# Performance work log

Measured on AMD Instinct MI355X. Metric: run time of the kernel, lower is better.

Reference implementation:

```python
import jax, jax.numpy as jnp
import numpy as np
import math

ALPHA = math.exp(-0.001 * 1000.0)  # exp(-dt * tau_filter_inv)
T, B, D_IN, D_OUT = 2048, 32, 512, 512


def setup_inputs() -> dict:
    key = jax.random.key(0)
    k1, k2, k3 = jax.random.split(key, 3)
    bound = 1.0 / math.sqrt(D_IN)  # torch Linear default init range
    return {
        "input_tensor": jax.random.normal(k1, (T, B, D_IN), dtype=jnp.float32),
        "weight": jax.random.uniform(k2, (D_OUT, D_IN), minval=-bound, maxval=bound, dtype=jnp.float32),
        "bias": jax.random.uniform(k3, (D_OUT,), minval=-bound, maxval=bound, dtype=jnp.float32),
    }


def reference(input_tensor, weight, bias):
    # y[t] = W x[t] + b   -> [T, B, D_OUT]
    y = jnp.einsum("tbi,oi->tbo", input_tensor, weight) + bias
    alpha = jnp.asarray(ALPHA, dtype=y.dtype)

    # out[0] = y[0]; out[t] = alpha * out[t-1] + y[t]
    def step(carry, yt):
        out = alpha * carry + yt
        return out, out

    _, rest = jax.lax.scan(step, y[0], y[1:])
    return jnp.concatenate([y[:1], rest], axis=0)
```

## Files before the change

kernel.cpp:

```cpp
#include <hip/hip_runtime.h>
#include <stdint.h>

#define T_DIM 2048
#define B_DIM 32
#define DIN   512
#define DOUT  512
#define M_DIM (T_DIM * B_DIM)
#define COLS  (B_DIM * DIN)
#define COLS4 (COLS / 4)

#define ALPHA_F 0.36787944117144233f
#define INV_1MA 1.5819767068693265f

#define CHUNKS   128
#define CHUNK_T  16
#define HALO     8

#define FCHUNKS  32
#define FCHUNK_T 64
#define FHALO    16

typedef float  floatx4 __attribute__((ext_vector_type(4)));
typedef __bf16 bf16x8  __attribute__((ext_vector_type(8)));

__device__ __forceinline__ uint32_t pk2(float a, float b) {
  uint32_t ua = __float_as_uint(a); ua += 0x7fffu + ((ua >> 16) & 1u);
  uint32_t ub = __float_as_uint(b); ub += 0x7fffu + ((ub >> 16) & 1u);
  return (ua >> 16) | (ub & 0xffff0000u);
}

__device__ __forceinline__ void gload_lds16(const void* g, void* lds) {
  __builtin_amdgcn_global_load_lds(
      (const __attribute__((address_space(1))) void*)g,
      (__attribute__((address_space(3))) void*)lds,
      16, 0, 0);
}

__device__ __forceinline__ void fma4(float4& c, const float4& v) {
  c.x = fmaf(ALPHA_F, c.x, v.x);
  c.y = fmaf(ALPHA_F, c.y, v.y);
  c.z = fmaf(ALPHA_F, c.z, v.z);
  c.w = fmaf(ALPHA_F, c.w, v.w);
}

__global__ void wconv_kernel(const float* __restrict__ W,
                             uint16_t* __restrict__ WB)
{
  const int t = blockIdx.x * 256 + threadIdx.x;
  const float4* W4 = (const float4*)W;
#pragma unroll
  for (int j = 0; j < 8; ++j) {
    const int b4 = t * 16 + j * 2;
    float4 w0 = W4[b4], w1 = W4[b4 + 1];
    uint4 p;
    p.x = pk2(w0.x, w0.y); p.y = pk2(w0.z, w0.w);
    p.z = pk2(w1.x, w1.y); p.w = pk2(w1.z, w1.w);
    *(uint4*)&WB[t * 64 + j * 8] = p;
  }
}

__global__ void filter_x_kernel(const float* __restrict__ X,
                                uint16_t* __restrict__ XF)
{
  const int col8 = blockIdx.x * 256 + threadIdx.x;
  const int c = blockIdx.y;
  const float4* X4 = (const float4*)X;

  const size_t cbase = (size_t)c * CHUNK_T * COLS4 + col8 * 2;

  float4 ca = {0.0f, 0.0f, 0.0f, 0.0f};
  float4 cb = {0.0f, 0.0f, 0.0f, 0.0f};

  if (c > 0) {
    float4 h[2 * HALO];
    const size_t hb = cbase - (size_t)HALO * COLS4;
#pragma unroll
    for (int j = 0; j < HALO; ++j) {
      h[2 * j]     = X4[hb + (size_t)j * COLS4];
      h[2 * j + 1] = X4[hb + (size_t)j * COLS4 + 1];
    }
#pragma unroll
    for (int j = 0; j < HALO; ++j) {
      fma4(ca, h[2 * j]);
      fma4(cb, h[2 * j + 1]);
    }
  }

  float4 cur[8], nxt[8];
#pragma unroll
  for (int j = 0; j < 4; ++j) {
    cur[2 * j]     = X4[cbase + (size_t)j * COLS4];
    cur[2 * j + 1] = X4[cbase + (size_t)j * COLS4 + 1];
  }
#pragma unroll
  for (int g = 0; g < 4; ++g) {
    if (g < 3) {
      const size_t nb = cbase + (size_t)((g + 1) * 4) * COLS4;
#pragma unroll
      for (int j = 0; j < 4; ++j) {
        nxt[2 * j]     = X4[nb + (size_t)j * COLS4];
        nxt[2 * j + 1] = X4[nb + (size_t)j * COLS4 + 1];
      }
    }
#pragma unroll
    for (int j = 0; j < 4; ++j) {
      fma4(ca, cur[2 * j]);
      fma4(cb, cur[2 * j + 1]);
      uint4 p;
      p.x = pk2(ca.x, ca.y); p.y = pk2(ca.z, ca.w);
      p.z = pk2(cb.x, cb.y); p.w = pk2(cb.z, cb.w);
      *(uint4*)&XF[(cbase + (size_t)(g * 4 + j) * COLS4) * 4] = p;
    }
#pragma unroll
    for (int j = 0; j < 8; ++j) cur[j] = nxt[j];
  }
}

__launch_bounds__(256, 4)
__global__ void gemm_bf16_kernel(const uint16_t* __restrict__ XF,
                                 const uint16_t* __restrict__ WB,
                                 const float* __restrict__ bias,
                                 float* __restrict__ Y)
{
  __shared__ __align__(16) uint16_t As[128 * 64];
  __shared__ __align__(16) uint16_t Bs[128 * 64];

  const int bid = blockIdx.x;
  const int lg = (bid & 7) * 256 + (bid >> 3);
  const int n0 = (lg & 3) * 128;
  const int m0 = (lg >> 2) * 128;

  const int tid  = threadIdx.x;
  const int lane = tid & 63;
  const int w    = tid >> 6;
  const int r    = lane & 15;
  const int q    = lane >> 4;
  const int wm   = w >> 1;
  const int wn   = w & 1;

  const int srow_base = w * 32 + (lane >> 3);
  const int schunk    = lane & 7;

  floatx4 acc[4][4];
#pragma unroll
  for (int i = 0; i < 4; ++i)
#pragma unroll
    for (int j = 0; j < 4; ++j) {
      floatx4 z = {0.0f, 0.0f, 0.0f, 0.0f};
      acc[i][j] = z;
    }

  for (int kt = 0; kt < DIN / 64; ++kt) {
    const int k0 = kt * 64;
#pragma unroll
    for (int i = 0; i < 4; ++i) {
      const int row = srow_base + i * 8;
      const int sc = schunk ^ (row & 7);
      gload_lds16(XF + (size_t)(m0 + row) * DIN + k0 + sc * 8,
                  &As[(w * 32 + i * 8) * 64]);
      gload_lds16(WB + (size_t)(n0 + row) * DIN + k0 + sc * 8,
                  &Bs[(w * 32 + i * 8) * 64]);
    }
    __syncthreads();

#pragma unroll
    for (int kk = 0; kk < 2; ++kk) {
      bf16x8 af[4], bfr[4];
#pragma unroll
      for (int mi = 0; mi < 4; ++mi) {
        const int row = wm * 64 + mi * 16 + r;
        const int cch = (kk * 4 + q) ^ (row & 7);
        af[mi] = *(const bf16x8*)&As[row * 64 + (cch << 3)];
      }
#pragma unroll
      for (int ni = 0; ni < 4; ++ni) {
        const int row = wn * 64 + ni * 16 + r;
        const int cch = (kk * 4 + q) ^ (row & 7);
        bfr[ni] = *(const bf16x8*)&Bs[row * 64 + (cch << 3)];
      }
#pragma unroll
      for (int mi = 0; mi < 4; ++mi)
#pragma unroll
        for (int ni = 0; ni < 4; ++ni)
          acc[mi][ni] = __builtin_amdgcn_mfma_f32_16x16x32_bf16(
              af[mi], bfr[ni], acc[mi][ni], 0, 0, 0);
    }
    __syncthreads();
  }

#pragma unroll
  for (int mi = 0; mi < 4; ++mi) {
    const int rowb = m0 + wm * 64 + mi * 16;
    const int t = rowb >> 5;
    const float s = (1.0f - __expf(-(float)(t + 1))) * INV_1MA;
#pragma unroll
    for (int ni = 0; ni < 4; ++ni) {
      const int col = n0 + wn * 64 + ni * 16 + r;
      const float sb = s * bias[col];
#pragma unroll
      for (int j = 0; j < 4; ++j)
        Y[(size_t)(rowb + q * 4 + j) * DOUT + col] = acc[mi][ni][j] + sb;
    }
  }
}

__launch_bounds__(256, 2)
__global__ void gemm_bias_kernel(const float* __restrict__ X,
                                 const float* __restrict__ W,
                                 const float* __restrict__ bias,
                                 float* __restrict__ Y,
                                 float* __restrict__ halo,
                                 int halo_on)
{
  __shared__ __align__(16) uint16_t As[128 * 64];
  __shared__ __align__(16) uint16_t Bs[128 * 64];

  const int tid  = threadIdx.x;
  const int lane = tid & 63;
  const int wave = tid >> 6;
  const int wm   = wave >> 1;
  const int wn   = wave & 1;
  const int r    = lane & 15;
  const int q    = lane >> 4;

  const int m0 = blockIdx.y * 128;
  const int n0 = blockIdx.x * 128;

  floatx4 acc[4][4];
#pragma unroll
  for (int i = 0; i < 4; ++i)
#pragma unroll
    for (int j = 0; j < 4; ++j) {
      floatx4 z = {0.0f, 0.0f, 0.0f, 0.0f};
      acc[i][j] = z;
    }

  for (int kt = 0; kt < DIN / 64; ++kt) {
    const int k0 = kt * 64;
#pragma unroll
    for (int j = 0; j < 4; ++j) {
      const int cid = tid + j * 256;
      const int row = cid >> 3;
      const int c   = cid & 7;
      const int slot = (c ^ (row & 7)) << 3;

      const float* ga = &X[(size_t)(m0 + row) * DIN + k0 + c * 8];
      float4 a0 = *(const float4*)ga;
      float4 a1 = *(const float4*)(ga + 4);
      uint4 pa;
      pa.x = pk2(a0.x, a0.y); pa.y = pk2(a0.z, a0.w);
      pa.z = pk2(a1.x, a1.y); pa.w = pk2(a1.z, a1.w);
      *(uint4*)&As[row * 64 + slot] = pa;

      const float* gb = &W[(size_t)(n0 + row) * DIN + k0 + c * 8];
      float4 b0 = *(const float4*)gb;
      float4 b1 = *(const float4*)(gb + 4);
      uint4 pb;
      pb.x = pk2(b0.x, b0.y); pb.y = pk2(b0.z, b0.w);
      pb.z = pk2(b1.x, b1.y); pb.w = pk2(b1.z, b1.w);
      *(uint4*)&Bs[row * 64 + slot] = pb;
    }
    __syncthreads();

#pragma unroll
    for (int kk = 0; kk < 2; ++kk) {
      bf16x8 af[4], bfr[4];
#pragma unroll
      for (int mi = 0; mi < 4; ++mi) {
        const int row = wm * 64 + mi * 16 + r;
        const int c   = (kk * 4 + q) ^ (row & 7);
        af[mi] = *(const bf16x8*)&As[row * 64 + (c << 3)];
      }
#pragma unroll
      for (int ni = 0; ni < 4; ++ni) {
        const int row = wn * 64 + ni * 16 + r;
        const int c   = (kk * 4 + q) ^ (row & 7);
        bfr[ni] = *(const bf16x8*)&Bs[row * 64 + (c << 3)];
      }
#pragma unroll
      for (int mi = 0; mi < 4; ++mi)
#pragma unroll
        for (int ni = 0; ni < 4; ++ni)
          acc[mi][ni] = __builtin_amdgcn_mfma_f32_16x16x32_bf16(
              af[mi], bfr[ni], acc[mi][ni], 0, 0, 0);
    }
    __syncthreads();
  }

#pragma unroll
  for (int ni = 0; ni < 4; ++ni) {
    const int col = n0 + wn * 64 + ni * 16 + r;
    const float bv = bias[col];
#pragma unroll
    for (int mi = 0; mi < 4; ++mi) {
      const int rowm = m0 + wm * 64 + mi * 16 + q * 4;
      const int t = rowm >> 5;
      const int b = rowm & 31;
      const int tloc = t & (FCHUNK_T - 1);
      const bool hw = halo_on && (tloc >= FCHUNK_T - FHALO) && (t < T_DIM - FCHUNK_T);
      const size_t hbase = hw
          ? ((size_t)(((t >> 6) + 1) * FHALO + (tloc - (FCHUNK_T - FHALO))) * COLS)
          : 0;
#pragma unroll
      for (int j = 0; j < 4; ++j) {
        const float v = acc[mi][ni][j] + bv;
        Y[(size_t)(rowm + j) * DOUT + col] = v;
        if (hw) halo[hbase + (size_t)(b + j) * DOUT + col] = v;
      }
    }
  }
}

__global__ void scan_kernel(float* __restrict__ Y,
                            const float* __restrict__ halo,
                            int chunk_len)
{
  const int col4 = blockIdx.x * blockDim.x + threadIdx.x;
  const int c = blockIdx.y;

  float4* Y4 = (float4*)Y;
  const float4* H4 = (const float4*)halo;

  float4 carry = {0.0f, 0.0f, 0.0f, 0.0f};
  if (c > 0) {
#pragma unroll
    for (int h = 0; h < FHALO; ++h) {
      float4 v = H4[(size_t)(c * FHALO + h) * COLS4 + col4];
      fma4(carry, v);
    }
  }

  size_t idx = (size_t)c * chunk_len * COLS4 + col4;
  float4 ynext = Y4[idx];
  for (int t = 0; t < chunk_len; ++t) {
    float4 y = ynext;
    if (t + 1 < chunk_len) ynext = Y4[idx + COLS4];
    fma4(carry, y);
    Y4[idx] = carry;
    idx += COLS4;
  }
}

extern "C" void kernel_launch(void* const* d_in, const int* in_sizes, int n_in,
                              void* d_out, int out_size, void* d_ws, size_t ws_size,
                              hipStream_t stream)
{
  const float* X    = (const float*)d_in[0];
  const float* W    = (const float*)d_in[1];
  const float* bias = (const float*)d_in[2];
  float* Y = (float*)d_out;

  const size_t need_new = (size_t)M_DIM * DIN * 2 + (size_t)DOUT * DIN * 2;

  if (ws_size >= need_new) {
    uint16_t* XF = (uint16_t*)d_ws;
    uint16_t* WB = XF + (size_t)M_DIM * DIN;

    wconv_kernel<<<16, 256, 0, stream>>>(W, WB);
    dim3 gf(8, CHUNKS);
    filter_x_kernel<<<gf, 256, 0, stream>>>(X, XF);
    gemm_bf16_kernel<<<2048, 256, 0, stream>>>(XF, WB, bias, Y);
  } else {
    float* halo = (float*)d_ws;
    const size_t halo_need = (size_t)FCHUNKS * FHALO * COLS * sizeof(float);
    const int halo_on = (ws_size >= halo_need) ? 1 : 0;

    dim3 g1(DOUT / 128, M_DIM / 128);
    gemm_bias_kernel<<<g1, 256, 0, stream>>>(X, W, bias, Y, halo, halo_on);

    const int n_chunks = halo_on ? FCHUNKS : 1;
    dim3 g2(COLS4 / 256, n_chunks);
    scan_kernel<<<g2, 256, 0, stream>>>(Y, halo, T_DIM / n_chunks);
  }
}
```

Before: 107.6 us.

## Fuse input filtering into GEMM with per-batch time slabs

Replaces the separate filter pass (which wrote a bf16 filtered copy of X to workspace) and the GEMM with one fused kernel. Each block handles one batch index and a 256-step time slab: it filters X into a full-K LDS tile of 128 rows, then sweeps all output columns with double-buffered weight tiles. This removes the global write and re-read of the filtered intermediate. In exchange it uses only 256 blocks with one block per CU because of the large LDS footprint, and each thread issues strided X loads, so occupancy and latency hiding may suffer.

```diff
diff --git a/kernel.cpp b/kernel.cpp
--- a/kernel.cpp
+++ b/kernel.cpp
@@ -12,9 +12,9 @@
 #define ALPHA_F 0.36787944117144233f
 #define INV_1MA 1.5819767068693265f
 
-#define CHUNKS   128
-#define CHUNK_T  16
-#define HALO     8
+#define HALO   8
+#define TSLAB  256
+#define NSLABS 8
 
 #define FCHUNKS  32
 #define FCHUNK_T 64
@@ -59,76 +59,19 @@
   }
 }
 
-__global__ void filter_x_kernel(const float* __restrict__ X,
-                                uint16_t* __restrict__ XF)
-{
-  const int col8 = blockIdx.x * 256 + threadIdx.x;
-  const int c = blockIdx.y;
-  const float4* X4 = (const float4*)X;
-
-  const size_t cbase = (size_t)c * CHUNK_T * COLS4 + col8 * 2;
-
-  float4 ca = {0.0f, 0.0f, 0.0f, 0.0f};
-  float4 cb = {0.0f, 0.0f, 0.0f, 0.0f};
-
-  if (c > 0) {
-    float4 h[2 * HALO];
-    const size_t hb = cbase - (size_t)HALO * COLS4;
-#pragma unroll
-    for (int j = 0; j < HALO; ++j) {
-      h[2 * j]     = X4[hb + (size_t)j * COLS4];
-      h[2 * j + 1] = X4[hb + (size_t)j * COLS4 + 1];
-    }
-#pragma unroll
-    for (int j = 0; j < HALO; ++j) {
-      fma4(ca, h[2 * j]);
-      fma4(cb, h[2 * j + 1]);
-    }
-  }
-
-  float4 cur[8], nxt[8];
-#pragma unroll
-  for (int j = 0; j < 4; ++j) {
-    cur[2 * j]     = X4[cbase + (size_t)j * COLS4];
-    cur[2 * j + 1] = X4[cbase + (size_t)j * COLS4 + 1];
-  }
-#pragma unroll
-  for (int g = 0; g < 4; ++g) {
-    if (g < 3) {
-      const size_t nb = cbase + (size_t)((g + 1) * 4) * COLS4;
-#pragma unroll
-      for (int j = 0; j < 4; ++j) {
-        nxt[2 * j]     = X4[nb + (size_t)j * COLS4];
-        nxt[2 * j + 1] = X4[nb + (size_t)j * COLS4 + 1];
-      }
-    }
-#pragma unroll
-    for (int j = 0; j < 4; ++j) {
-      fma4(ca, cur[2 * j]);
-      fma4(cb, cur[2 * j + 1]);
-      uint4 p;
-      p.x = pk2(ca.x, ca.y); p.y = pk2(ca.z, ca.w);
-      p.z = pk2(cb.x, cb.y); p.w = pk2(cb.z, cb.w);
-      *(uint4*)&XF[(cbase + (size_t)(g * 4 + j) * COLS4) * 4] = p;
-    }
-#pragma unroll
-    for (int j = 0; j < 8; ++j) cur[j] = nxt[j];
-  }
-}
-
-__launch_bounds__(256, 4)
-__global__ void gemm_bf16_kernel(const uint16_t* __restrict__ XF,
-                                 const uint16_t* __restrict__ WB,
-                                 const float* __restrict__ bias,
-                                 float* __restrict__ Y)
-{
-  __shared__ __align__(16) uint16_t As[128 * 64];
-  __shared__ __align__(16) uint16_t Bs[128 * 64];
-
-  const int bid = blockIdx.x;
-  const int lg = (bid & 7) * 256 + (bid >> 3);
-  const int n0 = (lg & 3) * 128;
-  const int m0 = (lg >> 2) * 128;
+__launch_bounds__(256, 1)
+__global__ void fused_bslab_kernel(const float* __restrict__ X,
+                                   const uint16_t* __restrict__ WB,
+                                   const float* __restrict__ bias,
+                                   float* __restrict__ Y)
+{
+  __shared__ __align__(16) uint16_t As[128 * 512];
+  __shared__ __align__(16) uint16_t Bs[2][128 * 64];
+
+  const int bid  = blockIdx.x;
+  const int b_   = bid & 31;
+  const int slab = bid >> 5;
+  const int tbase = slab * TSLAB;
 
   const int tid  = threadIdx.x;
   const int lane = tid & 63;
@@ -138,68 +81,142 @@
   const int wm   = w >> 1;
   const int wn   = w & 1;
 
+  const int k16 = tid & 127;
+  const int th  = tid >> 7;
+
   const int srow_base = w * 32 + (lane >> 3);
   const int schunk    = lane & 7;
 
+  const float4* X4 = (const float4*)X;
+  const float4 zero4 = {0.0f, 0.0f, 0.0f, 0.0f};
+
+#pragma unroll
+  for (int i = 0; i < 4; ++i) {
+    const int row = srow_base + i * 8;
+    const int sc = schunk ^ (row & 7);
+    gload_lds16(WB + (size_t)row * DIN + sc * 8,
+                &Bs[0][(w * 32 + i * 8) * 64]);
+  }
+
   floatx4 acc[4][4];
-#pragma unroll
-  for (int i = 0; i < 4; ++i)
-#pragma unroll
-    for (int j = 0; j < 4; ++j) {
-      floatx4 z = {0.0f, 0.0f, 0.0f, 0.0f};
-      acc[i][j] = z;
-    }
-
-  for (int kt = 0; kt < DIN / 64; ++kt) {
-    const int k0 = kt * 64;
-#pragma unroll
-    for (int i = 0; i < 4; ++i) {
-      const int row = srow_base + i * 8;
-      const int sc = schunk ^ (row & 7);
-      gload_lds16(XF + (size_t)(m0 + row) * DIN + k0 + sc * 8,
-                  &As[(w * 32 + i * 8) * 64]);
-      gload_lds16(WB + (size_t)(n0 + row) * DIN + k0 + sc * 8,
-                  &Bs[(w * 32 + i * 8) * 64]);
-    }
+  float sv[16];
+
+  for (int sub = 0; sub < 2; ++sub) {
+    const int t0 = tbase + sub * 128 + th * 64;
+    float4 va[8], vb[8];
+    float4 ca = {0.0f, 0.0f, 0.0f, 0.0f};
+
+#pragma unroll
+    for (int j = 0; j < 8; ++j) {
+      const int t = t0 - 8 + j;
+      va[j] = (t >= 0) ? X4[(size_t)t * 4096 + (size_t)b_ * 128 + k16] : zero4;
+    }
+#pragma unroll
+    for (int j = 0; j < 8; ++j)
+      vb[j] = X4[(size_t)(t0 + j) * 4096 + (size_t)b_ * 128 + k16];
+#pragma unroll
+    for (int j = 0; j < 8; ++j) fma4(ca, va[j]);
+
+#pragma unroll
+    for (int g = 0; g < 8; ++g) {
+      float4* cu = (g & 1) ? va : vb;
+      float4* nx = (g & 1) ? vb : va;
+      if (g < 7) {
+#pragma unroll
+        for (int j = 0; j < 8; ++j)
+          nx[j] = X4[(size_t)(t0 + (g + 1) * 8 + j) * 4096 + (size_t)b_ * 128 + k16];
+      }
+#pragma unroll
+      for (int j = 0; j < 8; ++j) {
+        fma4(ca, cu[j]);
+        const int row  = th * 64 + g * 8 + j;
+        const int slot = (k16 >> 1) ^ (row & 7);
+        uint2 p;
+        p.x = pk2(ca.x, ca.y);
+        p.y = pk2(ca.z, ca.w);
+        *(uint2*)&As[row * 512 + slot * 8 + (k16 & 1) * 4] = p;
+      }
+    }
+
+#pragma unroll
+    for (int mi = 0; mi < 4; ++mi)
+#pragma unroll
+      for (int j = 0; j < 4; ++j) {
+        const int tg = tbase + sub * 128 + wm * 64 + mi * 16 + q * 4 + j;
+        sv[mi * 4 + j] = (1.0f - __expf(-(float)(tg + 1))) * INV_1MA;
+      }
+
     __syncthreads();
 
-#pragma unroll
-    for (int kk = 0; kk < 2; ++kk) {
-      bf16x8 af[4], bfr[4];
-#pragma unroll
-      for (int mi = 0; mi < 4; ++mi) {
-        const int row = wm * 64 + mi * 16 + r;
-        const int cch = (kk * 4 + q) ^ (row & 7);
-        af[mi] = *(const bf16x8*)&As[row * 64 + (cch << 3)];
-      }
-#pragma unroll
-      for (int ni = 0; ni < 4; ++ni) {
-        const int row = wn * 64 + ni * 16 + r;
-        const int cch = (kk * 4 + q) ^ (row & 7);
-        bfr[ni] = *(const bf16x8*)&Bs[row * 64 + (cch << 3)];
-      }
-#pragma unroll
-      for (int mi = 0; mi < 4; ++mi)
-#pragma unroll
-        for (int ni = 0; ni < 4; ++ni)
-          acc[mi][ni] = __builtin_amdgcn_mfma_f32_16x16x32_bf16(
-              af[mi], bfr[ni], acc[mi][ni], 0, 0, 0);
-    }
-    __syncthreads();
-  }
-
-#pragma unroll
-  for (int mi = 0; mi < 4; ++mi) {
-    const int rowb = m0 + wm * 64 + mi * 16;
-    const int t = rowb >> 5;
-    const float s = (1.0f - __expf(-(float)(t + 1))) * INV_1MA;
-#pragma unroll
-    for (int ni = 0; ni < 4; ++ni) {
-      const int col = n0 + wn * 64 + ni * 16 + r;
-      const float sb = s * bias[col];
-#pragma unroll
-      for (int j = 0; j < 4; ++j)
-        Y[(size_t)(rowb + q * 4 + j) * DOUT + col] = acc[mi][ni][j] + sb;
+    for (int c = 0; c < 32; ++c) {
+      const int nt = c >> 3;
+      const int kc = c & 7;
+      const int cb = c & 1;
+
+      if (!(sub == 1 && c == 31)) {
+        const int cn  = (c + 1) & 31;
+        const int nnt = cn >> 3;
+        const int nkc = cn & 7;
+#pragma unroll
+        for (int i = 0; i < 4; ++i) {
+          const int row = srow_base + i * 8;
+          const int sc = schunk ^ (row & 7);
+          gload_lds16(WB + (size_t)(nnt * 128 + row) * DIN + nkc * 64 + sc * 8,
+                      &Bs[cb ^ 1][(w * 32 + i * 8) * 64]);
+        }
+      }
+
+      if (kc == 0) {
+#pragma unroll
+        for (int i = 0; i < 4; ++i)
+#pragma unroll
+          for (int j2 = 0; j2 < 4; ++j2) {
+            floatx4 z = {0.0f, 0.0f, 0.0f, 0.0f};
+            acc[i][j2] = z;
+          }
+      }
+
+#pragma unroll
+      for (int kk = 0; kk < 2; ++kk) {
+        bf16x8 af[4], bfr[4];
+#pragma unroll
+        for (int mi = 0; mi < 4; ++mi) {
+          const int row  = wm * 64 + mi * 16 + r;
+          const int slot = (kc * 8 + kk * 4 + q) ^ (row & 7);
+          af[mi] = *(const bf16x8*)&As[row * 512 + slot * 8];
+        }
+#pragma unroll
+        for (int ni = 0; ni < 4; ++ni) {
+          const int row = wn * 64 + ni * 16 + r;
+          const int cch = (kk * 4 + q) ^ (row & 7);
+          bfr[ni] = *(const bf16x8*)&Bs[cb][row * 64 + cch * 8];
+        }
+#pragma unroll
+        for (int mi = 0; mi < 4; ++mi)
+#pragma unroll
+          for (int ni = 0; ni < 4; ++ni)
+            acc[mi][ni] = __builtin_amdgcn_mfma_f32_16x16x32_bf16(
+                af[mi], bfr[ni], acc[mi][ni], 0, 0, 0);
+      }
+
+      if (kc == 7) {
+#pragma unroll
+        for (int ni = 0; ni < 4; ++ni) {
+          const int col = nt * 128 + wn * 64 + ni * 16 + r;
+          const float bv = bias[col];
+#pragma unroll
+          for (int mi = 0; mi < 4; ++mi) {
+#pragma unroll
+            for (int j = 0; j < 4; ++j) {
+              const int tg = tbase + sub * 128 + wm * 64 + mi * 16 + q * 4 + j;
+              Y[(size_t)tg * 16384 + (size_t)b_ * 512 + col] =
+                  acc[mi][ni][j] + sv[mi * 4 + j] * bv;
+            }
+          }
+        }
+      }
+
+      __syncthreads();
     }
   }
 }
@@ -213,7 +230,7 @@
                                  int halo_on)
 {
   __shared__ __align__(16) uint16_t As[128 * 64];
-  __shared__ __align__(16) uint16_t Bs[128 * 64];
+  __shared__ __align__(16) uint16_t Bsh[128 * 64];
 
   const int tid  = threadIdx.x;
   const int lane = tid & 63;
@@ -258,7 +275,7 @@
       uint4 pb;
       pb.x = pk2(b0.x, b0.y); pb.y = pk2(b0.z, b0.w);
       pb.z = pk2(b1.x, b1.y); pb.w = pk2(b1.z, b1.w);
-      *(uint4*)&Bs[row * 64 + slot] = pb;
+      *(uint4*)&Bsh[row * 64 + slot] = pb;
     }
     __syncthreads();
 
@@ -275,7 +292,7 @@
       for (int ni = 0; ni < 4; ++ni) {
         const int row = wn * 64 + ni * 16 + r;
         const int c   = (kk * 4 + q) ^ (row & 7);
-        bfr[ni] = *(const bf16x8*)&Bs[row * 64 + (c << 3)];
+        bfr[ni] = *(const bf16x8*)&Bsh[row * 64 + (c << 3)];
       }
 #pragma unroll
       for (int mi = 0; mi < 4; ++mi)
@@ -350,16 +367,12 @@
   const float* bias = (const float*)d_in[2];
   float* Y = (float*)d_out;
 
-  const size_t need_new = (size_t)M_DIM * DIN * 2 + (size_t)DOUT * DIN * 2;
-
-  if (ws_size >= need_new) {
-    uint16_t* XF = (uint16_t*)d_ws;
-    uint16_t* WB = XF + (size_t)M_DIM * DIN;
-
+  const size_t need_wb = (size_t)DOUT * DIN * 2;
+
+  if (ws_size >= need_wb) {
+    uint16_t* WB = (uint16_t*)d_ws;
     wconv_kernel<<<16, 256, 0, stream>>>(W, WB);
-    dim3 gf(8, CHUNKS);
-    filter_x_kernel<<<gf, 256, 0, stream>>>(X, XF);
-    gemm_bf16_kernel<<<2048, 256, 0, stream>>>(XF, WB, bias, Y);
+    fused_bslab_kernel<<<B_DIM * NSLABS, 256, 0, stream>>>(X, WB, bias, Y);
   } else {
     float* halo = (float*)d_ws;
     const size_t halo_need = (size_t)FCHUNKS * FHALO * COLS * sizeof(float);
```

Result: slower. 126.3 us (+17.4%).
